# Optimization experiments

Measured on AMD Instinct MI355X. Metric: run time of the kernel, lower is better.

## Reference

```python
import jax, jax.numpy as jnp
import numpy as np
import math

B_SZ, T_LEN, DIM = 1, 1024, 1024
D_STATE, EXPAND, NUM_SCALES, CONV_K = 16, 2, 3, 4
D_INNER = EXPAND * DIM
EPS_LOG = 1e-38
LN_EPS = 1e-5


def _causal_dwconv(x, w, b):
    # x: (B,T,D), w: (D,1,K) depthwise, b: (D,). torch Conv1d(pad=K-1)[:, :, :T] == left-pad K-1 (causal).
    y = jax.lax.conv_general_dilated(
        jnp.transpose(x, (0, 2, 1)), w, window_strides=(1,),
        padding=[(CONV_K - 1, 0)], dimension_numbers=('NCH', 'OIH', 'NCH'),
        feature_group_count=w.shape[0])
    return jnp.transpose(y, (0, 2, 1)) + b


def _ssm_core(x, cw, cb, xw, dtw, dtb, Dp):
    # x: (B,T,d_inner)
    xc = jax.nn.silu(_causal_dwconv(x, cw, cb))
    proj = xc @ xw.T                               # (B,T,2*d_state)
    B_ssm, C_ssm = proj[..., :D_STATE], proj[..., D_STATE:]
    dt = jax.nn.softplus(B_ssm @ dtw.T + dtb)      # (B,T,d_inner)
    dt = jax.nn.softplus(dt)                       # selective_scan applies softplus a second time (faithful)
    A = -jnp.arange(1, D_STATE + 1, dtype=xc.dtype)  # (d_state,) == -A_init row, same for every d_inner channel
    dA = jnp.exp(dt[..., None] * A)                # (B,T,d_inner,d_state)
    dBx = dt[..., None] * B_ssm[:, :, None, :] * xc[..., None]
    log_dA = jnp.log(jnp.clip(dA, EPS_LOG))
    log_dBx = jnp.log(jnp.clip(dBx, EPS_LOG))
    # parallel_scan_cpu: h = exp(cumsum(log_dA) + logcumsumexp(log_dBx - cumsum(log_dA)))
    a_star = jnp.cumsum(log_dA, axis=1)
    h = jnp.exp(a_star + jax.lax.cumlogsumexp(log_dBx - a_star, axis=1))
    return jnp.einsum('bts,btds->btd', C_ssm, h) + Dp * xc


def _downsample(x, stride):
    if stride == 1:
        return x
    Bb, T, D = x.shape
    Tt = (T // stride) * stride
    return x[:, :Tt].reshape(Bb, Tt // stride, stride, D).mean(2)


def _upsample(x, T_out):
    # F.interpolate(mode='linear', align_corners=False)
    T_in = x.shape[1]
    if T_in == T_out:
        return x
    scale = T_in / T_out
    pos = jnp.clip((jnp.arange(T_out, dtype=jnp.float32) + 0.5) * scale - 0.5, 0.0, T_in - 1)
    lo = jnp.floor(pos).astype(jnp.int32)
    hi = jnp.minimum(lo + 1, T_in - 1)
    w = (pos - lo.astype(pos.dtype))[None, :, None]
    return x[:, lo] * (1.0 - w) + x[:, hi] * w


def _forward(x, in_proj_w, conv_w, conv_b, xproj_w, dtproj_w, dtproj_b,
             D_param, scale_weights, gate_w1, gate_w2, out_proj_w, ln_g, ln_b):
    residual = x
    xz = x @ in_proj_w.T                           # (B,T,2*d_inner)
    x_in, gate = xz[..., :D_INNER], xz[..., D_INNER:]
    outs = []
    for s in range(NUM_SCALES):
        x_s = _downsample(x_in, 2 ** s)
        y_s = _ssm_core(x_s, conv_w[s], conv_b[s], xproj_w[s], dtproj_w[s], dtproj_b[s], D_param[s])
        outs.append(_upsample(y_s, x.shape[1]))
    w = jax.nn.softmax(scale_weights)
    fused = sum(w[s] * outs[s] for s in range(NUM_SCALES))
    ctx = sum(outs) / NUM_SCALES
    gate_ctx = jax.nn.sigmoid(jax.nn.silu(ctx @ gate_w1.T) @ gate_w2.T)
    out = (fused * gate_ctx) * jax.nn.silu(gate)
    out = out @ out_proj_w.T
    y = out + residual
    mu = y.mean(-1, keepdims=True)
    var = ((y - mu) ** 2).mean(-1, keepdims=True)
    return (y - mu) / jnp.sqrt(var + LN_EPS) * ln_g + ln_b


def setup_inputs() -> dict:
    key = jax.random.key(0)
    ks = jax.random.split(key, 12)
    g = lambda k, shp, s: (jax.random.normal(k, shp, jnp.float32) * s)
    return {
        'x': g(ks[0], (B_SZ, T_LEN, DIM), 1.0),
        'in_proj_w': g(ks[1], (2 * D_INNER, DIM), DIM ** -0.5),
        'conv_w': g(ks[2], (NUM_SCALES, D_INNER, 1, CONV_K), CONV_K ** -0.5),
        'conv_b': g(ks[3], (NUM_SCALES, D_INNER), 0.02),
        'xproj_w': g(ks[4], (NUM_SCALES, 2 * D_STATE, D_INNER), D_INNER ** -0.5),
        'dtproj_w': g(ks[5], (NUM_SCALES, D_INNER, D_STATE), D_STATE ** -0.5),
        'dtproj_b': jax.random.uniform(ks[6], (NUM_SCALES, D_INNER), jnp.float32,
                                       math.log(0.001), math.log(0.1)),
        'D_param': jnp.ones((NUM_SCALES, D_INNER), jnp.float32),
        'scale_weights': jnp.ones((NUM_SCALES,), jnp.float32) / NUM_SCALES,
        'gate_w1': g(ks[7], (D_INNER // 2, D_INNER), D_INNER ** -0.5),
        'gate_w2': g(ks[8], (D_INNER, D_INNER // 2), (D_INNER // 2) ** -0.5),
        'out_proj_w': g(ks[9], (DIM, D_INNER), D_INNER ** -0.5),
        'ln_g': jnp.ones((DIM,), jnp.float32),
        'ln_b': jnp.zeros((DIM,), jnp.float32),
    }


def reference(x, in_proj_w, conv_w, conv_b, xproj_w, dtproj_w, dtproj_b,
              D_param, scale_weights, gate_w1, gate_w2, out_proj_w, ln_g, ln_b):
    return _forward(x, in_proj_w, conv_w, conv_b, xproj_w, dtproj_w, dtproj_b,
                    D_param, scale_weights, gate_w1, gate_w2, out_proj_w, ln_g, ln_b)
```

## Files before the change

kernel.cpp:

```cpp
#include <hip/hip_runtime.h>

typedef unsigned short u16;
typedef float floatx2 __attribute__((ext_vector_type(2)));
typedef float floatx4 __attribute__((ext_vector_type(4)));
typedef short shortx8 __attribute__((ext_vector_type(8)));

#define DIN 2048

__device__ __forceinline__ u16 f2bf(float f){
  unsigned u = __float_as_uint(f);
  u = (u + 0x7fffu + ((u>>16)&1u))>>16;
  return (u16)u;
}
__device__ __forceinline__ float sigf(float x){ return 1.f/(1.f+__expf(-x)); }
__device__ __forceinline__ float siluf(float x){ return x*sigf(x); }
__device__ __forceinline__ floatx2 max2(floatx2 a, floatx2 b){
  floatx2 r; r.x = fmaxf(a.x, b.x); r.y = fmaxf(a.y, b.y); return r;
}

#define OFF_WINP  0ull
#define OFF_WG1   8388608ull
#define OFF_WG2   12582912ull
#define OFF_WOP   16777216ull
#define OFF_XB    20971520ull
#define OFF_XIN   23068672ull
#define OFF_SGATE 31457280ull
#define OFF_X1    39845888ull
#define OFF_X2    44040192ull
#define OFF_XC0   46137344ull
#define OFF_XC1   54525952ull
#define OFF_FUSED 60817408ull
#define OFF_G3O   69206016ull
#define OFF_Y0    75497472ull
#define OFF_Y1    83886080ull
#define OFF_Y2    88080384ull
#define OFF_P0    90177536ull
#define OFF_P1    90308608ull
#define OFF_P2    90374144ull
#define OFF_PS    92274688ull
#define OFF_HINIT 121634816ull
#define OFF_CTXB  OFF_XC0
#define OFF_T1B   OFF_XC1
#define OFF_T1A0  OFF_XIN
#define OFF_T1A1  OFF_X1
#define OFF_YPA0  OFF_Y1
#define OFF_YPA1  (OFF_XC0 + 4194304ull)

__device__ __forceinline__ void gld_lds16(const void* g, void* l){
  __builtin_amdgcn_global_load_lds((const __attribute__((address_space(1))) unsigned*)g,
                                   (__attribute__((address_space(3))) unsigned*)l, 16, 0, 0);
}

__global__ __launch_bounds__(256) void cvt_kernel(
    const float* __restrict__ s0, u16* __restrict__ d0,
    const float* __restrict__ s1, u16* __restrict__ d1,
    const float* __restrict__ s2, u16* __restrict__ d2,
    const float* __restrict__ s3, u16* __restrict__ d3,
    const float* __restrict__ s4, u16* __restrict__ d4)
{
  int i = (blockIdx.x*256 + threadIdx.x)*4;
  const float* s; u16* d;
  if      (i <  4194304){ s=s0; d=d0; }
  else if (i <  6291456){ s=s1; d=d1; i -=  4194304; }
  else if (i <  8388608){ s=s2; d=d2; i -=  6291456; }
  else if (i < 10485760){ s=s3; d=d3; i -=  8388608; }
  else                  { s=s4; d=d4; i -= 10485760; }
  const float4 v = *(const float4*)(s + i);
  ushort4 o; o.x = f2bf(v.x); o.y = f2bf(v.y); o.z = f2bf(v.z); o.w = f2bf(v.w);
  *(ushort4*)(d + i) = o;
}

template<int MODE, int BM>
__global__ __launch_bounds__(256) void gemm_bt(
    const u16* __restrict__ A, const u16* __restrict__ B,
    int N, int K, int Ks,
    float* __restrict__ out_f, float* __restrict__ out_f2, u16* __restrict__ out_b,
    const float* __restrict__ ex0f, const float* __restrict__ ex1f,
    float* __restrict__ ex0, float* __restrict__ ex1)
{
  constexpr int NI = BM/32;
  constexpr int IP = BM/64;
  __shared__ u16 smA[2][BM*32];
  __shared__ u16 smB[2][BM*32];
  const int tid  = threadIdx.x;
  const int m0   = blockIdx.y * BM;
  const int n0   = blockIdx.x * BM;
  const int wv   = tid >> 6;
  const int lane = tid & 63;
  const int mw   = (wv >> 1) * (BM/2);
  const int nw   = (wv & 1) * (BM/2);
  const int quad = lane >> 4;
  const int l16  = lane & 15;
  const int srow = tid >> 2;
  const int scol = (tid & 3) * 8;

  floatx4 acc[NI][NI];
#pragma unroll
  for (int i=0;i<NI;i++)
#pragma unroll
    for (int j=0;j<NI;j++) acc[i][j] = (floatx4)0.f;

  const int kStart = blockIdx.z * Ks;
  const int kEnd   = kStart + Ks;

  auto stage = [&](int buf, int k0){
#pragma unroll
    for (int p=0;p<IP;p++){
      gld_lds16(A + (size_t)(m0 + p*64 + srow)*K + k0 + scol, &smA[buf][p*2048 + wv*512]);
      gld_lds16(B + (size_t)(n0 + p*64 + srow)*K + k0 + scol, &smB[buf][p*2048 + wv*512]);
    }
  };

  stage(0, kStart);
  int cur = 0;
  for (int k0 = kStart; k0 < kEnd; k0 += 32) {
    __syncthreads();
    if (k0 + 32 < kEnd) stage(cur^1, k0+32);
    shortx8 af[NI], bfr[NI];
#pragma unroll
    for (int i=0;i<NI;i++){
      af[i]  = *(const shortx8*)&smA[cur][(mw + i*16 + l16)*32 + quad*8];
      bfr[i] = *(const shortx8*)&smB[cur][(nw + i*16 + l16)*32 + quad*8];
    }
#pragma unroll
    for (int i=0;i<NI;i++)
#pragma unroll
      for (int j=0;j<NI;j++)
        acc[i][j] = __builtin_amdgcn_mfma_f32_16x16x32_bf16(af[i], bfr[j], acc[i][j], 0, 0, 0);
    cur ^= 1;
  }

#pragma unroll
  for (int i=0;i<NI;i++){
    const int mb = m0 + mw + i*16 + quad*4;
#pragma unroll
    for (int j=0;j<NI;j++){
      const int n = n0 + nw + j*16 + l16;
      const floatx4 v4 = acc[i][j];
      if (MODE == 0){
        if (n < 2048){
#pragma unroll
          for (int r=0;r<4;r++) out_f[(size_t)(mb+r)*2048 + n] = v4[r];
          ex0[(size_t)(mb>>1)*2048 + n]       = 0.5f*(v4[0]+v4[1]);
          ex0[(size_t)((mb>>1)+1)*2048 + n]   = 0.5f*(v4[2]+v4[3]);
          ex1[(size_t)(mb>>2)*2048 + n]       = 0.25f*(v4[0]+v4[1]+v4[2]+v4[3]);
        } else {
#pragma unroll
          for (int r=0;r<4;r++) out_f2[(size_t)(mb+r)*2048 + (n-2048)] = siluf(v4[r]);
        }
      } else if (MODE == 2){
#pragma unroll
        for (int r=0;r<4;r++){
          const size_t idx = (size_t)(mb+r)*N + n;
          out_b[idx] = f2bf(sigf(v4[r]) * ex0f[idx] * ex1f[idx]);
        }
      } else {
        float* dst = blockIdx.z ? out_f2 : out_f;
#pragma unroll
        for (int r=0;r<4;r++) dst[(size_t)(mb+r)*N + n] = v4[r];
      }
    }
  }
}

__global__ __launch_bounds__(256) void g2_epi(const float* __restrict__ a,
    const float* __restrict__ b, u16* __restrict__ o){
  const int i = (blockIdx.x*256 + threadIdx.x)*4;
  const float4 va = *(const float4*)(a+i);
  const float4 vb = *(const float4*)(b+i);
  ushort4 r;
  r.x = f2bf(siluf(va.x+vb.x)); r.y = f2bf(siluf(va.y+vb.y));
  r.z = f2bf(siluf(va.z+vb.z)); r.w = f2bf(siluf(va.w+vb.w));
  *(ushort4*)(o+i) = r;
}

__global__ __launch_bounds__(256) void xproj_kernel(const float* __restrict__ x0,
    const float* __restrict__ x1, const float* __restrict__ x2,
    const float* __restrict__ cw, const float* __restrict__ cb,
    const float* __restrict__ xw,
    float* __restrict__ p0, float* __restrict__ p1, float* __restrict__ p2){
  __shared__ float srow[DIN];
  const int b = blockIdx.x;
  const float* xs; float* proj; int s, t;
  if (b < 1024)      { s=0; t=b;       xs=x0; proj=p0; }
  else if (b < 1536) { s=1; t=b-1024;  xs=x1; proj=p1; }
  else               { s=2; t=b-1536;  xs=x2; proj=p2; }
  const int tid = threadIdx.x;
#pragma unroll
  for (int q=0;q<2;q++){
    const int k = (q*256 + tid)*4;
    float4 xv[4];
#pragma unroll
    for (int j=0;j<4;j++){
      const int tt = t - 3 + j;
      if (tt >= 0) xv[j] = *(const float4*)(xs + (size_t)tt*DIN + k);
      else { xv[j].x = 0.f; xv[j].y = 0.f; xv[j].z = 0.f; xv[j].w = 0.f; }
    }
    const float4 w0 = *(const float4*)(cw + ((size_t)(s*DIN) + k + 0)*4);
    const float4 w1 = *(const float4*)(cw + ((size_t)(s*DIN) + k + 1)*4);
    const float4 w2 = *(const float4*)(cw + ((size_t)(s*DIN) + k + 2)*4);
    const float4 w3 = *(const float4*)(cw + ((size_t)(s*DIN) + k + 3)*4);
    const float4 cb4 = *(const float4*)(cb + (size_t)(s*DIN) + k);
    float4 r;
    r.x = siluf(cb4.x + w0.x*xv[0].x + w0.y*xv[1].x + w0.z*xv[2].x + w0.w*xv[3].x);
    r.y = siluf(cb4.y + w1.x*xv[0].y + w1.y*xv[1].y + w1.z*xv[2].y + w1.w*xv[3].y);
    r.z = siluf(cb4.z + w2.x*xv[0].z + w2.y*xv[1].z + w2.z*xv[2].z + w2.w*xv[3].z);
    r.w = siluf(cb4.w + w3.x*xv[0].w + w3.y*xv[1].w + w3.z*xv[2].w + w3.w*xv[3].w);
    *(float4*)&srow[k] = r;
  }
  __syncthreads();
  const int i = tid >> 3;
  const int j = tid & 7;
  const float4* w4 = (const float4*)(xw + ((size_t)s*32 + i)*DIN);
  const float4* s4 = (const float4*)srow;
  float acc = 0.f;
#pragma unroll 8
  for (int c=0;c<64;c++){
    const float4 sv = s4[j + 8*c];
    const float4 wv = w4[j + 8*c];
    acc += sv.x*wv.x + sv.y*wv.y + sv.z*wv.z + sv.w*wv.w;
  }
  acc += __shfl_xor(acc,1); acc += __shfl_xor(acc,2); acc += __shfl_xor(acc,4);
  if (j == 0) proj[t*32 + i] = acc;
}

__global__ __launch_bounds__(128) void scan_p1(
    const float* __restrict__ x0, const float* __restrict__ x1, const float* __restrict__ x2,
    const float* __restrict__ p0, const float* __restrict__ p1, const float* __restrict__ p2,
    const float* __restrict__ cw, const float* __restrict__ cb,
    const float* __restrict__ dtw, const float* __restrict__ dtb,
    float2* __restrict__ PS)
{
  __shared__ float sproj[16*32];
  int b = blockIdx.x;
  const float *xs, *proj; int base, s;
  if (b < 1024)      { xs=x0; proj=p0; base=0;  s=0; }
  else if (b < 1536) { b-=1024; xs=x1; proj=p1; base=64; s=1; }
  else               { b-=1536; xs=x2; proj=p2; base=96; s=2; }
  const int chunk = b >> 4;
  const int tid   = threadIdx.x;
  const int d     = (b & 15)*128 + tid;
  const int t0    = chunk*16;
  {
    const int k = tid*4;
    *(float4*)&sproj[k] = *(const float4*)&proj[t0*32 + k];
  }
  __syncthreads();

  const float4 wc  = *(const float4*)(cw + ((size_t)(s*DIN) + d)*4);
  const float  cbv = cb[s*DIN + d];
  floatx2 w2[8];
  const floatx2* wr = (const floatx2*)(dtw + ((size_t)(s*DIN) + d)*16);
#pragma unroll
  for (int k=0;k<8;k++) w2[k] = wr[k];
  const float bias = dtb[s*DIN + d];
  const floatx2 eps2 = {1e-38f, 1e-38f};

  floatx2 H2[8];
#pragma unroll
  for (int k=0;k<8;k++) H2[k] = (floatx2)0.f;
  float S = 0.f;
  const float* xp = xs + d;
  float h0=0.f, h1=0.f, h2=0.f;
  if (chunk){
    h0 = xp[(size_t)(t0-3)*DIN];
    h1 = xp[(size_t)(t0-2)*DIN];
    h2 = xp[(size_t)(t0-1)*DIN];
  }
  for (int tt=0; tt<16; tt++){
    const float xv  = xp[(size_t)(t0+tt)*DIN];
    const float xcv = siluf(cbv + wc.x*h0 + wc.y*h1 + wc.z*h2 + wc.w*xv);
    h0=h1; h1=h2; h2=xv;
    const floatx2* Bp2 = (const floatx2*)&sproj[tt*32];
    floatx2 zz = (floatx2)0.f;
#pragma unroll
    for (int k=0;k<8;k++) zz += Bp2[k]*w2[k];
    float z = fminf(zz.x + zz.y + bias, 60.f);
    const float E     = __expf(z);
    const float denom = 2.f + E;
    const float e     = __builtin_amdgcn_rcpf(denom);
    const float dtv   = __logf(denom);
    S += dtv;
    const floatx2 c2  = {dtv*xcv, dtv*xcv};
    const floatx2 es  = {e*e, e*e};
    floatx2 ep2 = {e, e*e};
#pragma unroll
    for (int k=0;k<8;k++){
      const floatx2 dA  = max2(ep2, eps2);
      const floatx2 dBx = max2(c2*Bp2[k], eps2);
      H2[k] = dA*H2[k] + dBx;
      ep2 *= es;
    }
  }
  const float q = __expf(-S);
  const floatx2 qs = {q*q, q*q};
  floatx2 qp2 = {q, q*q};
  float2* o = PS + (size_t)(base+chunk)*32768 + d;
#pragma unroll
  for (int k=0;k<8;k++){
    float2 v0; v0.x = qp2.x; v0.y = H2[k].x; o[(size_t)(2*k  )*2048] = v0;
    float2 v1; v1.x = qp2.y; v1.y = H2[k].y; o[(size_t)(2*k+1)*2048] = v1;
    qp2 *= qs;
  }
}

__global__ __launch_bounds__(256) void scan_combine(const float2* __restrict__ PS,
                                                    float* __restrict__ Hinit){
  int id = blockIdx.x*256 + threadIdx.x;
  int base, C;
  if (id < 32768)      { base=0;  C=64; }
  else if (id < 65536) { id-=32768; base=64; C=32; }
  else                 { id-=65536; base=96; C=16; }
  const size_t off = (size_t)base*32768 + id;
  const float2* ps = PS + off;
  float* hi = Hinit + off;
  float H = 0.f;
  for (int c=0;c<C;c++){
    hi[(size_t)c*32768] = H;
    const float2 v = ps[(size_t)c*32768];
    H = v.x*H + v.y;
  }
}

__global__ __launch_bounds__(128) void scan_p2(
    const float* __restrict__ x0, const float* __restrict__ x1, const float* __restrict__ x2,
    const float* __restrict__ p0, const float* __restrict__ p1, const float* __restrict__ p2,
    const float* __restrict__ cw, const float* __restrict__ cb,
    const float* __restrict__ dtw, const float* __restrict__ dtb,
    const float* __restrict__ Hinit, const float* __restrict__ Dp_all,
    float* __restrict__ y0, float* __restrict__ y1, float* __restrict__ y2)
{
  __shared__ float sproj[16*32];
  int b = blockIdx.x;
  const float *xs, *proj; float* y; int base, s;
  if (b < 1024)      { xs=x0; proj=p0; y=y0; base=0;  s=0; }
  else if (b < 1536) { b-=1024; xs=x1; proj=p1; y=y1; base=64; s=1; }
  else               { b-=1536; xs=x2; proj=p2; y=y2; base=96; s=2; }
  const int chunk = b >> 4;
  const int tid   = threadIdx.x;
  const int d     = (b & 15)*128 + tid;
  const int t0    = chunk*16;
  {
    const int k = tid*4;
    *(float4*)&sproj[k] = *(const float4*)&proj[t0*32 + k];
  }
  __syncthreads();

  const float4 wc  = *(const float4*)(cw + ((size_t)(s*DIN) + d)*4);
  const float  cbv = cb[s*DIN + d];
  floatx2 w2[8];
  const floatx2* wr = (const floatx2*)(dtw + ((size_t)(s*DIN) + d)*16);
#pragma unroll
  for (int k=0;k<8;k++) w2[k] = wr[k];
  const float bias = dtb[s*DIN + d];

  floatx2 H2[8];
  const float* hi = Hinit + (size_t)(base+chunk)*32768 + d;
#pragma unroll
  for (int k=0;k<8;k++){
    H2[k].x = hi[(size_t)(2*k  )*2048];
    H2[k].y = hi[(size_t)(2*k+1)*2048];
  }
  const float Dv = Dp_all[s*DIN + d];
  const floatx2 eps2 = {1e-38f, 1e-38f};
  const float* xp = xs + d;
  float* yp = y + (size_t)t0*DIN + d;
  float h0=0.f, h1=0.f, h2=0.f;
  if (chunk){
    h0 = xp[(size_t)(t0-3)*DIN];
    h1 = xp[(size_t)(t0-2)*DIN];
    h2 = xp[(size_t)(t0-1)*DIN];
  }
  for (int tt=0; tt<16; tt++){
    const float xv  = xp[(size_t)(t0+tt)*DIN];
    const float xcv = siluf(cbv + wc.x*h0 + wc.y*h1 + wc.z*h2 + wc.w*xv);
    h0=h1; h1=h2; h2=xv;
    const floatx2* Bp2 = (const floatx2*)&sproj[tt*32];
    floatx2 zz = (floatx2)0.f;
#pragma unroll
    for (int k=0;k<8;k++) zz += Bp2[k]*w2[k];
    float z = fminf(zz.x + zz.y + bias, 60.f);
    const float E     = __expf(z);
    const float denom = 2.f + E;
    const float e     = __builtin_amdgcn_rcpf(denom);
    const float dtv   = __logf(denom);
    const floatx2 c2 = {dtv*xcv, dtv*xcv};
    const floatx2 es = {e*e, e*e};
    floatx2 ep2 = {e, e*e};
    floatx2 pacc2 = (floatx2)0.f;
#pragma unroll
    for (int k=0;k<8;k++){
      const floatx2 dA  = max2(ep2, eps2);
      const floatx2 dBx = max2(c2*Bp2[k], eps2);
      H2[k] = dA*H2[k] + dBx;
      pacc2 += Bp2[8+k]*H2[k];
      ep2 *= es;
    }
    yp[(size_t)tt*DIN] = pacc2.x + pacc2.y + Dv*xcv;
  }
}

__device__ __forceinline__ float ups_read(const float* __restrict__ ys, int Tin, int t, int d){
  const float scale = (float)Tin * (1.f/1024.f);
  float pos = ((float)t + 0.5f)*scale - 0.5f;
  pos = fminf(fmaxf(pos, 0.f), (float)(Tin-1));
  const int lo = (int)floorf(pos);
  const float w = pos - (float)lo;
  const int hi = min(lo+1, Tin-1);
  return ys[(size_t)lo*DIN + d]*(1.f-w) + ys[(size_t)hi*DIN + d]*w;
}

__global__ __launch_bounds__(256) void fuse_kernel(const float* __restrict__ y0,
    const float* __restrict__ y1, const float* __restrict__ y2,
    const float* __restrict__ sw, u16* __restrict__ ctxb, float* __restrict__ fused){
  const int idx = blockIdx.x*256 + threadIdx.x;
  const int t = idx >> 11, d = idx & 2047;
  const float w0r = sw[0], w1r = sw[1], w2r = sw[2];
  const float mx = fmaxf(w0r, fmaxf(w1r, w2r));
  float e0 = __expf(w0r-mx), e1 = __expf(w1r-mx), e2 = __expf(w2r-mx);
  const float inv = 1.f/(e0+e1+e2);
  e0 *= inv; e1 *= inv; e2 *= inv;
  const float o0 = y0[idx];
  const float o1 = ups_read(y1, 512, t, d);
  const float o2 = ups_read(y2, 256, t, d);
  fused[idx] = e0*o0 + e1*o1 + e2*o2;
  ctxb[idx]  = f2bf((o0+o1+o2)*(1.f/3.f));
}

__global__ __launch_bounds__(256) void ln_kernel(const float* __restrict__ ya,
    const float* __restrict__ yb, const float* __restrict__ xr,
    const float* __restrict__ g, const float* __restrict__ b, float* __restrict__ out){
  __shared__ float red[4];
  const int t = blockIdx.x;
  const size_t ro = (size_t)t*1024;
  float v[4];
  float s = 0.f;
#pragma unroll
  for (int i=0;i<4;i++){
    const int c = threadIdx.x + i*256;
    v[i] = ya[ro+c] + yb[ro+c] + xr[ro+c];
    s += v[i];
  }
  s += __shfl_xor(s,1); s += __shfl_xor(s,2); s += __shfl_xor(s,4);
  s += __shfl_xor(s,8); s += __shfl_xor(s,16); s += __shfl_xor(s,32);
  if ((threadIdx.x & 63) == 0) red[threadIdx.x>>6] = s;
  __syncthreads();
  const float mu = (red[0]+red[1]+red[2]+red[3]) * (1.f/1024.f);
  __syncthreads();
  float q = 0.f;
#pragma unroll
  for (int i=0;i<4;i++){ const float dd = v[i]-mu; q += dd*dd; }
  q += __shfl_xor(q,1); q += __shfl_xor(q,2); q += __shfl_xor(q,4);
  q += __shfl_xor(q,8); q += __shfl_xor(q,16); q += __shfl_xor(q,32);
  if ((threadIdx.x & 63) == 0) red[threadIdx.x>>6] = q;
  __syncthreads();
  const float rstd = rsqrtf((red[0]+red[1]+red[2]+red[3]) * (1.f/1024.f) + 1e-5f);
#pragma unroll
  for (int i=0;i<4;i++){
    const int c = threadIdx.x + i*256;
    out[ro + c] = (v[i]-mu)*rstd*g[c] + b[c];
  }
}

extern "C" void kernel_launch(void* const* d_in, const int* in_sizes, int n_in,
                              void* d_out, int out_size, void* d_ws, size_t ws_size,
                              hipStream_t stream) {
  const float* x     = (const float*)d_in[0];
  const float* inpw  = (const float*)d_in[1];
  const float* convw = (const float*)d_in[2];
  const float* convb = (const float*)d_in[3];
  const float* xpw   = (const float*)d_in[4];
  const float* dtw   = (const float*)d_in[5];
  const float* dtb   = (const float*)d_in[6];
  const float* Dp    = (const float*)d_in[7];
  const float* sw    = (const float*)d_in[8];
  const float* gw1   = (const float*)d_in[9];
  const float* gw2   = (const float*)d_in[10];
  const float* opw   = (const float*)d_in[11];
  const float* lng   = (const float*)d_in[12];
  const float* lnb   = (const float*)d_in[13];
  float* out = (float*)d_out;

  char* ws = (char*)d_ws;
  u16*    wInp  = (u16*)   (ws + OFF_WINP);
  u16*    wG1   = (u16*)   (ws + OFF_WG1);
  u16*    wG2   = (u16*)   (ws + OFF_WG2);
  u16*    wOp   = (u16*)   (ws + OFF_WOP);
  u16*    xb    = (u16*)   (ws + OFF_XB);
  float*  xin   = (float*) (ws + OFF_XIN);
  float*  sgate = (float*) (ws + OFF_SGATE);
  float*  x1    = (float*) (ws + OFF_X1);
  float*  x2    = (float*) (ws + OFF_X2);
  float*  y0    = (float*) (ws + OFF_Y0);
  float*  y1    = (float*) (ws + OFF_Y1);
  float*  y2    = (float*) (ws + OFF_Y2);
  float*  p0    = (float*) (ws + OFF_P0);
  float*  p1    = (float*) (ws + OFF_P1);
  float*  p2    = (float*) (ws + OFF_P2);
  float2* PS    = (float2*)(ws + OFF_PS);
  float*  Hinit = (float*) (ws + OFF_HINIT);
  u16*    ctxb  = (u16*)   (ws + OFF_CTXB);
  u16*    t1b   = (u16*)   (ws + OFF_T1B);
  float*  fused = (float*) (ws + OFF_FUSED);
  u16*    g3o   = (u16*)   (ws + OFF_G3O);
  float*  t1a0  = (float*) (ws + OFF_T1A0);
  float*  t1a1  = (float*) (ws + OFF_T1A1);
  float*  ypa0  = (float*) (ws + OFF_YPA0);
  float*  ypa1  = (float*) (ws + OFF_YPA1);

  cvt_kernel<<<11264, 256, 0, stream>>>(inpw, wInp, gw1, wG1, gw2, wG2, opw, wOp, x, xb);
  gemm_bt<0,64><<<dim3(64, 16, 1), 256, 0, stream>>>(xb, wInp, 4096, 1024, 1024,
                                                     xin, sgate, nullptr, nullptr, nullptr, x1, x2);
  xproj_kernel<<<1792, 256, 0, stream>>>(xin, x1, x2, convw, convb, xpw, p0, p1, p2);
  scan_p1<<<1792, 128, 0, stream>>>(xin, x1, x2, p0, p1, p2, convw, convb, dtw, dtb, PS);
  scan_combine<<<384, 256, 0, stream>>>(PS, Hinit);
  scan_p2<<<1792, 128, 0, stream>>>(xin, x1, x2, p0, p1, p2, convw, convb, dtw, dtb,
                                    Hinit, Dp, y0, y1, y2);
  fuse_kernel<<<(1024*DIN)/256, 256, 0, stream>>>(y0, y1, y2, sw, ctxb, fused);
  gemm_bt<4,64><<<dim3(16, 16, 2), 256, 0, stream>>>(ctxb, wG1, 1024, 2048, 1024,
                                                     t1a0, t1a1, nullptr, nullptr, nullptr, nullptr, nullptr);
  g2_epi<<<1024, 256, 0, stream>>>(t1a0, t1a1, t1b);
  gemm_bt<2,64><<<dim3(32, 16, 1), 256, 0, stream>>>(t1b, wG2, 2048, 1024, 1024,
                                                     nullptr, nullptr, g3o, fused, sgate, nullptr, nullptr);
  gemm_bt<4,64><<<dim3(16, 16, 2), 256, 0, stream>>>(g3o, wOp, 1024, 2048, 1024,
                                                     ypa0, ypa1, nullptr, nullptr, nullptr, nullptr, nullptr);
  ln_kernel<<<1024, 256, 0, stream>>>(ypa0, ypa1, x, lng, lnb, out);
}
```

Baseline: 281.9 us.

## Drop split-K in gate/out GEMMs, fuse SiLU epilogue, store scan S instead of decay powers

Removes the split-K (z=2) partial-sum path for the gate1 and out-proj GEMMs and runs each over the full K, so the g2_epi kernel goes away and SiLU plus the bf16 conversion move into a new GEMM epilogue mode. The LayerNorm kernel now reads one partial buffer instead of two. The in_proj GEMM switches to a 128-wide tile variant with half the grid. The chunked scan now writes the per-chunk dt sum S and the chunk states separately, and the combine kernel recomputes each decay factor with exp, which cuts the bytes written and read for the chunk summaries. In exchange the GEMMs launch far fewer workgroups, which may leave many CUs idle on a 256-CU part.

```diff
diff --git a/kernel.cpp b/kernel.cpp
--- a/kernel.cpp
+++ b/kernel.cpp
@@ -37,14 +37,12 @@
 #define OFF_P0    90177536ull
 #define OFF_P1    90308608ull
 #define OFF_P2    90374144ull
-#define OFF_PS    92274688ull
+#define OFF_HC    92274688ull
 #define OFF_HINIT 121634816ull
+#define OFF_SARR  136314880ull
 #define OFF_CTXB  OFF_XC0
 #define OFF_T1B   OFF_XC1
-#define OFF_T1A0  OFF_XIN
-#define OFF_T1A1  OFF_X1
-#define OFF_YPA0  OFF_Y1
-#define OFF_YPA1  (OFF_XC0 + 4194304ull)
+#define OFF_YPA   OFF_Y1
 
 __device__ __forceinline__ void gld_lds16(const void* g, void* l){
   __builtin_amdgcn_global_load_lds((const __attribute__((address_space(1))) unsigned*)g,
@@ -154,6 +152,12 @@
           const size_t idx = (size_t)(mb+r)*N + n;
           out_b[idx] = f2bf(sigf(v4[r]) * ex0f[idx] * ex1f[idx]);
         }
+      } else if (MODE == 3){
+#pragma unroll
+        for (int r=0;r<4;r++){
+          const size_t idx = (size_t)(mb+r)*N + n;
+          out_b[idx] = f2bf(siluf(v4[r]));
+        }
       } else {
         float* dst = blockIdx.z ? out_f2 : out_f;
 #pragma unroll
@@ -161,17 +165,6 @@
       }
     }
   }
-}
-
-__global__ __launch_bounds__(256) void g2_epi(const float* __restrict__ a,
-    const float* __restrict__ b, u16* __restrict__ o){
-  const int i = (blockIdx.x*256 + threadIdx.x)*4;
-  const float4 va = *(const float4*)(a+i);
-  const float4 vb = *(const float4*)(b+i);
-  ushort4 r;
-  r.x = f2bf(siluf(va.x+vb.x)); r.y = f2bf(siluf(va.y+vb.y));
-  r.z = f2bf(siluf(va.z+vb.z)); r.w = f2bf(siluf(va.w+vb.w));
-  *(ushort4*)(o+i) = r;
 }
 
 __global__ __launch_bounds__(256) void xproj_kernel(const float* __restrict__ x0,
@@ -229,7 +222,7 @@
     const float* __restrict__ p0, const float* __restrict__ p1, const float* __restrict__ p2,
     const float* __restrict__ cw, const float* __restrict__ cb,
     const float* __restrict__ dtw, const float* __restrict__ dtb,
-    float2* __restrict__ PS)
+    float* __restrict__ Sarr, float* __restrict__ Hc)
 {
   __shared__ float sproj[16*32];
   int b = blockIdx.x;
@@ -292,33 +285,33 @@
       ep2 *= es;
     }
   }
-  const float q = __expf(-S);
-  const floatx2 qs = {q*q, q*q};
-  floatx2 qp2 = {q, q*q};
-  float2* o = PS + (size_t)(base+chunk)*32768 + d;
+  Sarr[(size_t)(base+chunk)*2048 + d] = S;
+  float* o = Hc + (size_t)(base+chunk)*32768 + d;
 #pragma unroll
   for (int k=0;k<8;k++){
-    float2 v0; v0.x = qp2.x; v0.y = H2[k].x; o[(size_t)(2*k  )*2048] = v0;
-    float2 v1; v1.x = qp2.y; v1.y = H2[k].y; o[(size_t)(2*k+1)*2048] = v1;
-    qp2 *= qs;
-  }
-}
-
-__global__ __launch_bounds__(256) void scan_combine(const float2* __restrict__ PS,
-                                                    float* __restrict__ Hinit){
+    o[(size_t)(2*k  )*2048] = H2[k].x;
+    o[(size_t)(2*k+1)*2048] = H2[k].y;
+  }
+}
+
+__global__ __launch_bounds__(256) void scan_combine(const float* __restrict__ Sarr,
+    const float* __restrict__ Hc, float* __restrict__ Hinit){
   int id = blockIdx.x*256 + threadIdx.x;
   int base, C;
   if (id < 32768)      { base=0;  C=64; }
   else if (id < 65536) { id-=32768; base=64; C=32; }
   else                 { id-=65536; base=96; C=16; }
+  const int n = id >> 11, d = id & 2047;
+  const float fn = -(float)(n+1);
   const size_t off = (size_t)base*32768 + id;
-  const float2* ps = PS + off;
+  const float* hc = Hc + off;
   float* hi = Hinit + off;
+  const float* sp = Sarr + (size_t)base*2048 + d;
   float H = 0.f;
   for (int c=0;c<C;c++){
     hi[(size_t)c*32768] = H;
-    const float2 v = ps[(size_t)c*32768];
-    H = v.x*H + v.y;
+    const float e = __expf(fn * sp[(size_t)c*2048]);
+    H = e*H + hc[(size_t)c*32768];
   }
 }
 
@@ -428,7 +421,7 @@
 }
 
 __global__ __launch_bounds__(256) void ln_kernel(const float* __restrict__ ya,
-    const float* __restrict__ yb, const float* __restrict__ xr,
+    const float* __restrict__ xr,
     const float* __restrict__ g, const float* __restrict__ b, float* __restrict__ out){
   __shared__ float red[4];
   const int t = blockIdx.x;
@@ -438,7 +431,7 @@
 #pragma unroll
   for (int i=0;i<4;i++){
     const int c = threadIdx.x + i*256;
-    v[i] = ya[ro+c] + yb[ro+c] + xr[ro+c];
+    v[i] = ya[ro+c] + xr[ro+c];
     s += v[i];
   }
   s += __shfl_xor(s,1); s += __shfl_xor(s,2); s += __shfl_xor(s,4);
@@ -497,32 +490,29 @@
   float*  p0    = (float*) (ws + OFF_P0);
   float*  p1    = (float*) (ws + OFF_P1);
   float*  p2    = (float*) (ws + OFF_P2);
-  float2* PS    = (float2*)(ws + OFF_PS);
+  float*  Sarr  = (float*) (ws + OFF_SARR);
+  float*  Hc    = (float*) (ws + OFF_HC);
   float*  Hinit = (float*) (ws + OFF_HINIT);
   u16*    ctxb  = (u16*)   (ws + OFF_CTXB);
   u16*    t1b   = (u16*)   (ws + OFF_T1B);
   float*  fused = (float*) (ws + OFF_FUSED);
   u16*    g3o   = (u16*)   (ws + OFF_G3O);
-  float*  t1a0  = (float*) (ws + OFF_T1A0);
-  float*  t1a1  = (float*) (ws + OFF_T1A1);
-  float*  ypa0  = (float*) (ws + OFF_YPA0);
-  float*  ypa1  = (float*) (ws + OFF_YPA1);
+  float*  ypa   = (float*) (ws + OFF_YPA);
 
   cvt_kernel<<<11264, 256, 0, stream>>>(inpw, wInp, gw1, wG1, gw2, wG2, opw, wOp, x, xb);
-  gemm_bt<0,64><<<dim3(64, 16, 1), 256, 0, stream>>>(xb, wInp, 4096, 1024, 1024,
+  gemm_bt<0,128><<<dim3(32, 8, 1), 256, 0, stream>>>(xb, wInp, 4096, 1024, 1024,
                                                      xin, sgate, nullptr, nullptr, nullptr, x1, x2);
   xproj_kernel<<<1792, 256, 0, stream>>>(xin, x1, x2, convw, convb, xpw, p0, p1, p2);
-  scan_p1<<<1792, 128, 0, stream>>>(xin, x1, x2, p0, p1, p2, convw, convb, dtw, dtb, PS);
-  scan_combine<<<384, 256, 0, stream>>>(PS, Hinit);
+  scan_p1<<<1792, 128, 0, stream>>>(xin, x1, x2, p0, p1, p2, convw, convb, dtw, dtb, Sarr, Hc);
+  scan_combine<<<384, 256, 0, stream>>>(Sarr, Hc, Hinit);
   scan_p2<<<1792, 128, 0, stream>>>(xin, x1, x2, p0, p1, p2, convw, convb, dtw, dtb,
                                     Hinit, Dp, y0, y1, y2);
   fuse_kernel<<<(1024*DIN)/256, 256, 0, stream>>>(y0, y1, y2, sw, ctxb, fused);
-  gemm_bt<4,64><<<dim3(16, 16, 2), 256, 0, stream>>>(ctxb, wG1, 1024, 2048, 1024,
-                                                     t1a0, t1a1, nullptr, nullptr, nullptr, nullptr, nullptr);
-  g2_epi<<<1024, 256, 0, stream>>>(t1a0, t1a1, t1b);
+  gemm_bt<3,64><<<dim3(16, 16, 1), 256, 0, stream>>>(ctxb, wG1, 1024, 2048, 2048,
+                                                     nullptr, nullptr, t1b, nullptr, nullptr, nullptr, nullptr);
   gemm_bt<2,64><<<dim3(32, 16, 1), 256, 0, stream>>>(t1b, wG2, 2048, 1024, 1024,
                                                      nullptr, nullptr, g3o, fused, sgate, nullptr, nullptr);
-  gemm_bt<4,64><<<dim3(16, 16, 2), 256, 0, stream>>>(g3o, wOp, 1024, 2048, 1024,
-                                                     ypa0, ypa1, nullptr, nullptr, nullptr, nullptr, nullptr);
-  ln_kernel<<<1024, 256, 0, stream>>>(ypa0, ypa1, x, lng, lnb, out);
-}
+  gemm_bt<4,64><<<dim3(16, 16, 1), 256, 0, stream>>>(g3o, wOp, 1024, 2048, 2048,
+                                                     ypa, nullptr, nullptr, nullptr, nullptr, nullptr, nullptr);
+  ln_kernel<<<1024, 256, 0, stream>>>(ypa, x, lng, lnb, out);
+}
```

After: 303.6 us. 7.7% more time.
